# Optimization experiments

Measured on AMD Instinct MI355X. Metric: run time of the kernel, lower is better.

## Reference

```python
import jax, jax.numpy as jnp
import numpy as np
import math

N_STOCKS, SEQ_T, D_FEAT, D_MODEL = 1024, 32, 158, 256
H_T, H_S = 4, 4
MAX_LEN = 100
LN_EPS = 1e-5


def _make_pe():
    # PositionalEncoding buffer, identical to the torch construction
    pos = np.arange(MAX_LEN, dtype=np.float32)[:, None]
    div = np.exp(np.arange(0, D_MODEL, 2, dtype=np.float32) * (-math.log(10000.0) / D_MODEL))
    pe = np.zeros((MAX_LEN, D_MODEL), dtype=np.float32)
    pe[:, 0::2] = np.sin(pos * div)
    pe[:, 1::2] = np.cos(pos * div)
    return jnp.asarray(pe)


def _ln(x, g, b):
    mu = x.mean(-1, keepdims=True)
    var = ((x - mu) ** 2).mean(-1, keepdims=True)
    return (x - mu) / jnp.sqrt(var + LN_EPS) * g + b


def _mha(q, k, v, nhead, scale):
    # q,k,v: [B,S,D]; full (non-causal) attention over S, vectorized over heads
    B, S, D = q.shape
    hd = D // nhead
    qh = q.reshape(B, S, nhead, hd)
    kh = k.reshape(B, S, nhead, hd)
    vh = v.reshape(B, S, nhead, hd)
    scores = jnp.einsum('bqhd,bkhd->bhqk', qh, kh) * scale
    attn = jax.nn.softmax(scores, axis=-1)  # dropout is identity in eval
    out = jnp.einsum('bhqk,bkhd->bqhd', attn, vh)
    return out.reshape(B, S, D)


def _block(x, wq, wk, wv, g1, b1, g2, b2, w1, bb1, w2, bb2, nhead, scale, swap):
    # shared body of TAttention (swap=False, scale=1) / SAttention (swap=True, scale=1/temperature)
    xn = _ln(x, g1, b1)
    q, k, v = xn @ wq, xn @ wk, xn @ wv
    if swap:  # SAttention attends over the stock axis: transpose(0,1)
        q, k, v = q.swapaxes(0, 1), k.swapaxes(0, 1), v.swapaxes(0, 1)
    att = _mha(q, k, v, nhead, scale)
    if swap:
        att = att.swapaxes(0, 1)
    xt = _ln(xn + att, g2, b2)
    ffn = jax.nn.relu(xt @ w1 + bb1) @ w2 + bb2
    return xt + ffn


def _forward(x_enc, emb_w, emb_b, pe,
             t_wq, t_wk, t_wv, t_ln1_g, t_ln1_b, t_ln2_g, t_ln2_b, t_w1, t_b1, t_w2, t_b2,
             s_wq, s_wk, s_wv, s_ln1_g, s_ln1_b, s_ln2_g, s_ln2_b, s_w1, s_b1, s_w2, s_b2,
             ta_w, dec_w, dec_b):
    x = x_enc[0]  # squeeze(dim=0) -> [N, T, d_feat]
    h = x @ emb_w + emb_b + pe[:x.shape[1]]  # embedding + positional encoding
    # TAttention: attention over time axis, NO temperature scaling in source
    h = _block(h, t_wq, t_wk, t_wv, t_ln1_g, t_ln1_b, t_ln2_g, t_ln2_b,
               t_w1, t_b1, t_w2, t_b2, H_T, 1.0, swap=False)
    # SAttention: attention over stock axis, scaled by 1/sqrt(d_model/nhead)
    s_scale = 1.0 / math.sqrt(D_MODEL / H_S)
    h = _block(h, s_wq, s_wk, s_wv, s_ln1_g, s_ln1_b, s_ln2_g, s_ln2_b,
               s_w1, s_b1, s_w2, s_b2, H_S, s_scale, swap=True)
    # TemporalAttention: last-timestep query pooling over T
    hh = h @ ta_w                                  # [N,T,D]
    lam = jnp.einsum('ntd,nd->nt', hh, hh[:, -1, :])
    lam = jax.nn.softmax(lam, axis=1)
    pooled = jnp.einsum('nt,ntd->nd', lam, h)      # matmul(lam[:,None,:], z).squeeze(1)
    return pooled @ dec_w + dec_b                  # [N, 2]


def setup_inputs():
    key = jax.random.key(0)
    ks = iter(jax.random.split(key, 48))
    def w(shape, s=0.02):
        return jax.random.normal(next(ks), shape, dtype=jnp.float32) * s
    D = D_MODEL
    inp = {
        'x_enc': jax.random.normal(next(ks), (1, N_STOCKS, SEQ_T, D_FEAT), jnp.float32),
        'x_mark_enc': jax.random.normal(next(ks), (1, N_STOCKS, SEQ_T, 4), jnp.float32),
        'x_dec': jax.random.normal(next(ks), (1, SEQ_T, D_FEAT), jnp.float32),
        'x_mark_dec': jax.random.normal(next(ks), (1, SEQ_T, 4), jnp.float32),
        'x_tweet': jax.random.randint(next(ks), (1, 128), 0, 30000, dtype=jnp.int32),
        'emb_w': w((D_FEAT, D)), 'emb_b': jnp.zeros((D,), jnp.float32),
        'pe': _make_pe(),
        't_wq': w((D, D)), 't_wk': w((D, D)), 't_wv': w((D, D)),
        't_ln1_g': jnp.ones((D,), jnp.float32), 't_ln1_b': jnp.zeros((D,), jnp.float32),
        't_ln2_g': jnp.ones((D,), jnp.float32), 't_ln2_b': jnp.zeros((D,), jnp.float32),
        't_w1': w((D, D)), 't_b1': jnp.zeros((D,), jnp.float32),
        't_w2': w((D, D)), 't_b2': jnp.zeros((D,), jnp.float32),
        's_wq': w((D, D)), 's_wk': w((D, D)), 's_wv': w((D, D)),
        's_ln1_g': jnp.ones((D,), jnp.float32), 's_ln1_b': jnp.zeros((D,), jnp.float32),
        's_ln2_g': jnp.ones((D,), jnp.float32), 's_ln2_b': jnp.zeros((D,), jnp.float32),
        's_w1': w((D, D)), 's_b1': jnp.zeros((D,), jnp.float32),
        's_w2': w((D, D)), 's_b2': jnp.zeros((D,), jnp.float32),
        'ta_w': w((D, D)),
        'dec_w': w((D, 2)), 'dec_b': jnp.zeros((2,), jnp.float32),
    }
    return inp


def reference(x_enc, x_mark_enc, x_dec, x_mark_dec, x_tweet, emb_w, emb_b, pe,
              t_wq, t_wk, t_wv, t_ln1_g, t_ln1_b, t_ln2_g, t_ln2_b, t_w1, t_b1, t_w2, t_b2,
              s_wq, s_wk, s_wv, s_ln1_g, s_ln1_b, s_ln2_g, s_ln2_b, s_w1, s_b1, s_w2, s_b2,
              ta_w, dec_w, dec_b):
    # x_mark_enc feeds a throwaway fresh Linear whose output is never used;
    # x_dec / x_mark_dec / x_tweet are unused in the source forward.
    pred = _forward(x_enc, emb_w, emb_b, pe,
                    t_wq, t_wk, t_wv, t_ln1_g, t_ln1_b, t_ln2_g, t_ln2_b, t_w1, t_b1, t_w2, t_b2,
                    s_wq, s_wk, s_wv, s_ln1_g, s_ln1_b, s_ln2_g, s_ln2_b, s_w1, s_b1, s_w2, s_b2,
                    ta_w, dec_w, dec_b)
    # (tweet_pred, data_pred, cat_pred, align_loss) all alias data_pred / 0
    return (pred, pred, pred, jnp.float32(0.0))
```

## Files before the change

kernel.cpp:

```cpp
#include <hip/hip_runtime.h>
#include <hip/hip_bf16.h>
#include <math.h>

#define NS 1024
#define ST 32
#define DF 158
#define DM 256
#define KE 192
#define ROWS (NS*ST)
#define SZ ((size_t)ROWS*DM)
#define LN_EPS 1e-5f
#define LOG2E 1.44269504088896f

typedef __attribute__((ext_vector_type(8)))  __bf16 bf16x8;
typedef __attribute__((ext_vector_type(16))) float  f32x16;

__device__ __forceinline__ float wave_sum(float v) {
#pragma unroll
    for (int o = 32; o > 0; o >>= 1) v += __shfl_xor(v, o);
    return v;
}

__device__ __forceinline__ unsigned pkbf(float a, float b) {
    __hip_bfloat16 ha = __float2bfloat16(a), hb = __float2bfloat16(b);
    unsigned short ua, ub;
    __builtin_memcpy(&ua, &ha, 2); __builtin_memcpy(&ub, &hb, 2);
    return (unsigned)ua | ((unsigned)ub << 16);
}

__device__ __forceinline__ unsigned pkbf_fast(float a, float b) {
    unsigned ua = __float_as_uint(a) + 0x8000u;
    unsigned ub = __float_as_uint(b) + 0x8000u;
    return (ua >> 16) | (ub & 0xffff0000u);
}

__device__ __forceinline__ unsigned short sbf(float a) {
    return (unsigned short)((__float_as_uint(a) + 0x8000u) >> 16);
}

__device__ __forceinline__ float2 bf2x(unsigned u) {
    union { unsigned i; float f; } a, b;
    a.i = u << 16; b.i = u & 0xffff0000u;
    return make_float2(a.f, b.f);
}

__device__ __forceinline__ uint4 addpk(uint4 rv, const float* s) {
    float2 f0 = bf2x(rv.x), f1 = bf2x(rv.y), f2 = bf2x(rv.z), f3 = bf2x(rv.w);
    return make_uint4(pkbf_fast(f0.x + s[0], f0.y + s[1]),
                      pkbf_fast(f1.x + s[2], f1.y + s[3]),
                      pkbf_fast(f2.x + s[4], f2.y + s[5]),
                      pkbf_fast(f3.x + s[6], f3.y + s[7]));
}

__device__ __forceinline__ uint4 addbk(uint4 a, uint4 b) {
    float2 a0 = bf2x(a.x), a1 = bf2x(a.y), a2 = bf2x(a.z), a3 = bf2x(a.w);
    float2 b0 = bf2x(b.x), b1 = bf2x(b.y), b2 = bf2x(b.z), b3 = bf2x(b.w);
    return make_uint4(pkbf_fast(a0.x + b0.x, a0.y + b0.y),
                      pkbf_fast(a1.x + b1.x, a1.y + b1.y),
                      pkbf_fast(a2.x + b2.x, a2.y + b2.y),
                      pkbf_fast(a3.x + b3.x, a3.y + b3.y));
}

__global__ __launch_bounds__(256) void cvtx_k(const float* __restrict__ x,
        __hip_bfloat16* __restrict__ xb) {
    int r = blockIdx.x*8 + (threadIdx.x >> 5);
    int c = blockIdx.y*32 + (threadIdx.x & 31);
    float v = (c < DF) ? x[(size_t)r*DF + c] : 0.f;
    xb[(size_t)r*KE + c] = __float2bfloat16(v);
}

struct WPack { const float* s[11]; __hip_bfloat16* d[11]; };

__global__ __launch_bounds__(256) void cvtw_k(WPack wp) {
    const float* W = wp.s[blockIdx.z];
    __hip_bfloat16* Wt = wp.d[blockIdx.z];
    __shared__ float t[64][65];
    int bi = blockIdx.x*64, bj = blockIdx.y*64;
    int r = threadIdx.x >> 2, c0 = (threadIdx.x & 3) * 16;
#pragma unroll
    for (int i = 0; i < 16; i += 4) {
        float4 v = *(const float4*)(W + (size_t)(bi + r)*DM + bj + c0 + i);
        t[r][c0+i+0] = v.x; t[r][c0+i+1] = v.y;
        t[r][c0+i+2] = v.z; t[r][c0+i+3] = v.w;
    }
    __syncthreads();
    unsigned u[8];
#pragma unroll
    for (int i = 0; i < 8; ++i) u[i] = pkbf(t[c0+2*i][r], t[c0+2*i+1][r]);
    __hip_bfloat16* op = Wt + (size_t)(bj + r)*DM + bi + c0;
    *(uint4*)(op)     = make_uint4(u[0], u[1], u[2], u[3]);
    *(uint4*)(op + 8) = make_uint4(u[4], u[5], u[6], u[7]);
}

__global__ __launch_bounds__(192) void cvte_k(const float* __restrict__ W,
        __hip_bfloat16* __restrict__ Wt) {
    int n = blockIdx.x, t = threadIdx.x;
    float v = (t < DF) ? W[(size_t)t*DM + n] : 0.f;
    Wt[(size_t)n*KE + t] = __float2bfloat16(v);
}

__global__ __launch_bounds__(256) void ln_k(const __hip_bfloat16* __restrict__ a,
        const float* __restrict__ g, const float* __restrict__ be,
        __hip_bfloat16* __restrict__ outb) {
    int w = threadIdx.x >> 6, lane = threadIdx.x & 63;
    size_t r = (size_t)blockIdx.x*4 + w;
    uint2 raw = *(const uint2*)(a + r*DM + lane*4);
    float2 v01 = bf2x(raw.x), v23 = bf2x(raw.y);
    float mu = wave_sum(v01.x+v01.y+v23.x+v23.y) * (1.0f/DM);
    float c0 = v01.x-mu, c1 = v01.y-mu, c2 = v23.x-mu, c3 = v23.y-mu;
    float var = wave_sum(c0*c0 + c1*c1 + c2*c2 + c3*c3) * (1.0f/DM);
    float rs = rsqrtf(var + LN_EPS);
    float4 g4 = *(const float4*)(g + lane*4);
    float4 b4 = *(const float4*)(be + lane*4);
    float o0 = c0*rs*g4.x + b4.x, o1 = c1*rs*g4.y + b4.y;
    float o2 = c2*rs*g4.z + b4.z, o3 = c3*rs*g4.w + b4.w;
    *(uint2*)(outb + r*DM + lane*4) = make_uint2(pkbf_fast(o0, o1), pkbf_fast(o2, o3));
}

union __align__(16) GLds {
    struct { __hip_bfloat16 As[64*72]; __hip_bfloat16 Ws[128*72]; } s;
    __hip_bfloat16 Ob[64*136];
};

__global__ __launch_bounds__(256) void mgemm_k(const __hip_bfloat16* __restrict__ A,
        int sA, int nk, const __hip_bfloat16* __restrict__ Wt, int sW,
        const float* __restrict__ bias, const float* __restrict__ pe,
        const __hip_bfloat16* __restrict__ resid, float* __restrict__ Cf,
        __hip_bfloat16* __restrict__ Cb, int relu, int fmt, float scale, int fused) {
    __shared__ GLds gsm;
    const int tid = threadIdx.x;
    const int w = tid >> 6, lane = tid & 63;
    const int uh = lane >> 5, l31 = lane & 31;
    const int wm = (w >> 1)*32, wn = (w & 1)*64;
    const size_t m0 = (size_t)blockIdx.x*64;
    const int n0 = blockIdx.y*128;

    f32x16 acc[2];
#pragma unroll
    for (int nt = 0; nt < 2; ++nt)
#pragma unroll
        for (int r = 0; r < 16; ++r) acc[nt][r] = 0.f;

    const int ra = tid >> 2, ca = (tid & 3)*16;
    const int rw = tid >> 1, cw = (tid & 1)*32;
    const __hip_bfloat16* ap = A  + (m0 + ra)*sA + ca;
    const __hip_bfloat16* wp = Wt + (size_t)(n0 + rw)*sW + cw;
    uint4 pa0 = *(const uint4*)(ap), pa1 = *(const uint4*)(ap + 8);
    uint4 pw0 = *(const uint4*)(wp),      pw1 = *(const uint4*)(wp + 8);
    uint4 pw2 = *(const uint4*)(wp + 16), pw3 = *(const uint4*)(wp + 24);
    for (int kt = 0; kt < nk; ++kt) {
        __syncthreads();
        *(uint4*)&gsm.s.As[ra*72 + ca]     = pa0;
        *(uint4*)&gsm.s.As[ra*72 + ca + 8] = pa1;
        *(uint4*)&gsm.s.Ws[rw*72 + cw]      = pw0;
        *(uint4*)&gsm.s.Ws[rw*72 + cw + 8]  = pw1;
        *(uint4*)&gsm.s.Ws[rw*72 + cw + 16] = pw2;
        *(uint4*)&gsm.s.Ws[rw*72 + cw + 24] = pw3;
        __syncthreads();
        if (kt + 1 < nk) {
            int ko = (kt + 1)*64;
            pa0 = *(const uint4*)(ap + ko);      pa1 = *(const uint4*)(ap + ko + 8);
            pw0 = *(const uint4*)(wp + ko);      pw1 = *(const uint4*)(wp + ko + 8);
            pw2 = *(const uint4*)(wp + ko + 16); pw3 = *(const uint4*)(wp + ko + 24);
        }
#pragma unroll
        for (int ks = 0; ks < 4; ++ks) {
            bf16x8 a0 = *(const bf16x8*)&gsm.s.As[(wm + l31)*72      + ks*16 + uh*8];
            bf16x8 b0 = *(const bf16x8*)&gsm.s.Ws[(wn + l31)*72      + ks*16 + uh*8];
            bf16x8 b1 = *(const bf16x8*)&gsm.s.Ws[(wn + 32 + l31)*72 + ks*16 + uh*8];
            acc[0] = __builtin_amdgcn_mfma_f32_32x32x16_bf16(a0, b0, acc[0], 0, 0, 0);
            acc[1] = __builtin_amdgcn_mfma_f32_32x32x16_bf16(a0, b1, acc[1], 0, 0, 0);
        }
    }

    if (Cf) {
#pragma unroll
        for (int nt = 0; nt < 2; ++nt) {
            int colg = n0 + wn + nt*32 + l31;
            float bz = bias ? bias[colg] : 0.f;
#pragma unroll
            for (int r = 0; r < 16; ++r) {
                size_t mg = m0 + wm + (r & 3) + ((r >> 2) << 3) + 4*uh;
                float v = (acc[nt][r] + bz) * scale;
                if (pe)   v += pe[(mg & 31)*DM + colg];
                if (relu) v = fmaxf(v, 0.f);
                Cf[mg*DM + colg] = v;
            }
        }
    } else {
        __syncthreads();
#pragma unroll
        for (int nt = 0; nt < 2; ++nt) {
            int col = wn + nt*32 + l31;
            int colg = n0 + col;
            int c8  = fused ? (colg & 255) : colg;
            float sc = (fused && (colg >> 8)) ? 1.0f : scale;
            float bz = bias ? bias[c8] : 0.f;
#pragma unroll
            for (int r = 0; r < 16; ++r) {
                int mrow = wm + (r & 3) + ((r >> 2) << 3) + 4*uh;
                float v = (acc[nt][r] + bz) * sc;
                if (pe)   v += pe[((m0 + mrow) & 31)*DM + c8];
                if (relu) v = fmaxf(v, 0.f);
                *(unsigned short*)&gsm.Ob[mrow*136 + col] = sbf(v);
            }
        }
        __syncthreads();
        int m = tid >> 2;
        size_t mg = m0 + m;
#pragma unroll
        for (int i = 0; i < 4; ++i) {
            int ncol = ((tid & 3) + 4*i)*8;
            uint4 val = *(const uint4*)&gsm.Ob[m*136 + ncol];
            int colg = n0 + ncol;
            int seg = fused ? (colg >> 8) : 0;
            int c8  = fused ? (colg & 255) : colg;
            if (resid) val = addbk(val, *(const uint4*)(resid + mg*DM + c8));
            size_t oidx;
            if (fmt == 1)
                oidx = (size_t)((mg & 31)*4 + (c8 >> 6))*65536 + (mg >> 5)*64 + (c8 & 63);
            else if (fmt == 2)
                oidx = ((size_t)(c8 >> 6)*NS + (mg >> 5))*2048 + (mg & 31)*64 + (c8 & 63);
            else
                oidx = mg*DM + c8;
            *(uint4*)&(Cb + (size_t)seg*SZ)[oidx] = val;
        }
    }
}

union __align__(16) WLds { __hip_bfloat16 vt[64*40]; float ob[32*68]; };

__global__ __launch_bounds__(256) void attnT_k(const __hip_bfloat16* __restrict__ Q,
        const __hip_bfloat16* __restrict__ K, const __hip_bfloat16* __restrict__ V,
        const __hip_bfloat16* __restrict__ R, const float* __restrict__ g,
        const float* __restrict__ be, __hip_bfloat16* __restrict__ O) {
    __shared__ WLds sm4[4];
    __shared__ float redS[32][8];
    __shared__ float redQ[32][8];
    const int n = blockIdx.x;
    const int w = threadIdx.x >> 6, lane = threadIdx.x & 63;
    const int uh = lane >> 5, l31 = lane & 31;
    const size_t base = ((size_t)w*NS + n)*2048;

    bf16x8 kf[4], qf[4];
#pragma unroll
    for (int s = 0; s < 4; ++s) {
        kf[s] = *(const bf16x8*)(K + base + l31*64 + s*16 + uh*8);
        qf[s] = *(const bf16x8*)(Q + base + l31*64 + s*16 + uh*8);
    }
    __hip_bfloat16* vt = sm4[w].vt;
#pragma unroll
    for (int i = 0; i < 2; ++i) {
        int c = lane*2 + i;
        int dg = c >> 3, tg = c & 7;
        const ushort* vp = (const ushort*)(V + base + (tg*4)*64 + dg*4);
        ushort4 s0 = *(const ushort4*)(vp);
        ushort4 s1 = *(const ushort4*)(vp + 64);
        ushort4 s2 = *(const ushort4*)(vp + 128);
        ushort4 s3 = *(const ushort4*)(vp + 192);
        *(uint2*)&vt[(dg*4+0)*40 + tg*4] = make_uint2((unsigned)s0.x | ((unsigned)s1.x<<16),
                                                      (unsigned)s2.x | ((unsigned)s3.x<<16));
        *(uint2*)&vt[(dg*4+1)*40 + tg*4] = make_uint2((unsigned)s0.y | ((unsigned)s1.y<<16),
                                                      (unsigned)s2.y | ((unsigned)s3.y<<16));
        *(uint2*)&vt[(dg*4+2)*40 + tg*4] = make_uint2((unsigned)s0.z | ((unsigned)s1.z<<16),
                                                      (unsigned)s2.z | ((unsigned)s3.z<<16));
        *(uint2*)&vt[(dg*4+3)*40 + tg*4] = make_uint2((unsigned)s0.w | ((unsigned)s1.w<<16),
                                                      (unsigned)s2.w | ((unsigned)s3.w<<16));
    }

    f32x16 sa;
#pragma unroll
    for (int r = 0; r < 16; ++r) sa[r] = 0.f;
    sa = __builtin_amdgcn_mfma_f32_32x32x16_bf16(kf[0], qf[0], sa, 0, 0, 0);
    sa = __builtin_amdgcn_mfma_f32_32x32x16_bf16(kf[1], qf[1], sa, 0, 0, 0);
    sa = __builtin_amdgcn_mfma_f32_32x32x16_bf16(kf[2], qf[2], sa, 0, 0, 0);
    sa = __builtin_amdgcn_mfma_f32_32x32x16_bf16(kf[3], qf[3], sa, 0, 0, 0);

    float p[16], l = 0.f;
#pragma unroll
    for (int r = 0; r < 16; ++r) { p[r] = __builtin_amdgcn_exp2f(sa[r]); l += p[r]; }
    l += __shfl_xor(l, 32);

    bf16x8 pf[2];
#pragma unroll
    for (int s = 0; s < 2; ++s) {
        unsigned A0 = pkbf_fast(p[8*s+0], p[8*s+1]);
        unsigned A1 = pkbf_fast(p[8*s+2], p[8*s+3]);
        unsigned B0 = pkbf_fast(p[8*s+4], p[8*s+5]);
        unsigned B1 = pkbf_fast(p[8*s+6], p[8*s+7]);
        unsigned xA0 = (unsigned)__shfl_xor((int)A0, 32);
        unsigned xA1 = (unsigned)__shfl_xor((int)A1, 32);
        unsigned xB0 = (unsigned)__shfl_xor((int)B0, 32);
        unsigned xB1 = (unsigned)__shfl_xor((int)B1, 32);
        union { uint4 i; bf16x8 v; } cv;
        cv.i = make_uint4(uh ? xB0 : A0, uh ? xB1 : A1,
                          uh ? B0 : xA0, uh ? B1 : xA1);
        pf[s] = cv.v;
    }

    f32x16 oa[2];
#pragma unroll
    for (int c = 0; c < 2; ++c) {
#pragma unroll
        for (int r = 0; r < 16; ++r) oa[c][r] = 0.f;
        bf16x8 v0 = *(const bf16x8*)&vt[(c*32 + l31)*40 + uh*8];
        bf16x8 v1 = *(const bf16x8*)&vt[(c*32 + l31)*40 + 16 + uh*8];
        oa[c] = __builtin_amdgcn_mfma_f32_32x32x16_bf16(v0, pf[0], oa[c], 0, 0, 0);
        oa[c] = __builtin_amdgcn_mfma_f32_32x32x16_bf16(v1, pf[1], oa[c], 0, 0, 0);
    }

    float invl = 1.0f / l;
    float* ob = sm4[w].ob;
#pragma unroll
    for (int c = 0; c < 2; ++c)
#pragma unroll
        for (int r = 0; r < 16; ++r) {
            int d = (r & 3) + ((r >> 2) << 3) + 4*uh + 32*c;
            ob[l31*68 + d] = oa[c][r] * invl;
        }
    int t = lane >> 1, d0 = (lane & 1)*32;
    size_t gi = ((size_t)n*ST + t)*DM + w*64 + d0;
    float ps = 0.f, pq = 0.f;
#pragma unroll
    for (int i = 0; i < 4; ++i) {
        uint4 rv = *(const uint4*)(R + gi + 8*i);
        float* s = &ob[t*68 + d0 + 8*i];
        float2 f0 = bf2x(rv.x), f1 = bf2x(rv.y), f2 = bf2x(rv.z), f3 = bf2x(rv.w);
        float v0 = f0.x + s[0], v1 = f0.y + s[1], v2 = f1.x + s[2], v3 = f1.y + s[3];
        float v4 = f2.x + s[4], v5 = f2.y + s[5], v6 = f3.x + s[6], v7 = f3.y + s[7];
        s[0] = v0; s[1] = v1; s[2] = v2; s[3] = v3;
        s[4] = v4; s[5] = v5; s[6] = v6; s[7] = v7;
        ps += v0+v1+v2+v3+v4+v5+v6+v7;
        pq += v0*v0+v1*v1+v2*v2+v3*v3+v4*v4+v5*v5+v6*v6+v7*v7;
    }
    redS[t][w*2 + (lane & 1)] = ps;
    redQ[t][w*2 + (lane & 1)] = pq;
    __syncthreads();
    float s8 = 0.f, q8 = 0.f;
#pragma unroll
    for (int i = 0; i < 8; ++i) { s8 += redS[t][i]; q8 += redQ[t][i]; }
    float mu = s8*(1.0f/DM);
    float var = q8*(1.0f/DM) - mu*mu;
    float rcp = rsqrtf(var + LN_EPS);
#pragma unroll
    for (int i = 0; i < 4; ++i) {
        const float* s = &ob[t*68 + d0 + 8*i];
        int cg = w*64 + d0 + 8*i;
        float4 g0 = *(const float4*)(g + cg),  g1 = *(const float4*)(g + cg + 4);
        float4 b0 = *(const float4*)(be + cg), b1 = *(const float4*)(be + cg + 4);
        float o0 = (s[0]-mu)*rcp*g0.x + b0.x, o1 = (s[1]-mu)*rcp*g0.y + b0.y;
        float o2 = (s[2]-mu)*rcp*g0.z + b0.z, o3 = (s[3]-mu)*rcp*g0.w + b0.w;
        float o4 = (s[4]-mu)*rcp*g1.x + b1.x, o5 = (s[5]-mu)*rcp*g1.y + b1.y;
        float o6 = (s[6]-mu)*rcp*g1.z + b1.z, o7 = (s[7]-mu)*rcp*g1.w + b1.w;
        *(uint4*)(O + gi + 8*i) = make_uint4(pkbf_fast(o0, o1), pkbf_fast(o2, o3),
                                             pkbf_fast(o4, o5), pkbf_fast(o6, o7));
    }
}

union __align__(16) LdsS {
    struct { __hip_bfloat16 K[64*72]; __hip_bfloat16 Vt[64*72]; } s;
    float Ob[4][32*68];
};

__global__ __launch_bounds__(256) void attnS_k(const __hip_bfloat16* __restrict__ Qb,
        const __hip_bfloat16* __restrict__ Kb, const __hip_bfloat16* __restrict__ Vb,
        const __hip_bfloat16* __restrict__ R, __hip_bfloat16* __restrict__ O) {
    __shared__ LdsS sm;
    const int tt = blockIdx.x, h = blockIdx.y, qt = blockIdx.z;
    const int tid = threadIdx.x;
    const int w = tid >> 6, lane = tid & 63;
    const int uh = lane >> 5, l31 = lane & 31;
    const size_t hb = (size_t)(tt*4 + h)*65536;

    bf16x8 qf[4];
    {
        const __hip_bfloat16* qp = Qb + hb + (size_t)(qt*128 + w*32 + l31)*64 + 8*uh;
        qf[0] = *(const bf16x8*)(qp);
        qf[1] = *(const bf16x8*)(qp + 16);
        qf[2] = *(const bf16x8*)(qp + 32);
        qf[3] = *(const bf16x8*)(qp + 48);
    }

    f32x16 oa[2];
#pragma unroll
    for (int c = 0; c < 2; ++c)
#pragma unroll
        for (int r = 0; r < 16; ++r) oa[c][r] = 0.f;
    float lrun = 0.f;

    for (int kt = 0; kt < 16; ++kt) {
        __syncthreads();
        {
            const __hip_bfloat16* kb = Kb + hb + (size_t)kt*4096;
#pragma unroll
            for (int i = 0; i < 2; ++i) {
                int c = tid*2 + i;
                int j = c >> 3, col = (c & 7)*8;
                *(uint4*)&sm.s.K[j*72 + col] = *(const uint4*)(kb + c*8);
            }
        }
        {
            int j0 = (tid & 15)*4, cb = (tid >> 4)*4;
            const ushort* vp = (const ushort*)(Vb + hb + (size_t)(kt*64 + j0)*64 + cb);
            ushort4 s0 = *(const ushort4*)(vp);
            ushort4 s1 = *(const ushort4*)(vp + 64);
            ushort4 s2 = *(const ushort4*)(vp + 128);
            ushort4 s3 = *(const ushort4*)(vp + 192);
            *(uint2*)&sm.s.Vt[(cb+0)*72 + j0] = make_uint2((unsigned)s0.x | ((unsigned)s1.x<<16),
                                                           (unsigned)s2.x | ((unsigned)s3.x<<16));
            *(uint2*)&sm.s.Vt[(cb+1)*72 + j0] = make_uint2((unsigned)s0.y | ((unsigned)s1.y<<16),
                                                           (unsigned)s2.y | ((unsigned)s3.y<<16));
            *(uint2*)&sm.s.Vt[(cb+2)*72 + j0] = make_uint2((unsigned)s0.z | ((unsigned)s1.z<<16),
                                                           (unsigned)s2.z | ((unsigned)s3.z<<16));
            *(uint2*)&sm.s.Vt[(cb+3)*72 + j0] = make_uint2((unsigned)s0.w | ((unsigned)s1.w<<16),
                                                           (unsigned)s2.w | ((unsigned)s3.w<<16));
        }
        __syncthreads();

        f32x16 sa[2];
#pragma unroll
        for (int ct = 0; ct < 2; ++ct) {
            f32x16 a2;
#pragma unroll
            for (int r = 0; r < 16; ++r) a2[r] = 0.f;
            const __hip_bfloat16* kb = &sm.s.K[(ct*32 + l31)*72 + 8*uh];
            a2 = __builtin_amdgcn_mfma_f32_32x32x16_bf16(*(const bf16x8*)(kb +  0), qf[0], a2, 0, 0, 0);
            a2 = __builtin_amdgcn_mfma_f32_32x32x16_bf16(*(const bf16x8*)(kb + 16), qf[1], a2, 0, 0, 0);
            a2 = __builtin_amdgcn_mfma_f32_32x32x16_bf16(*(const bf16x8*)(kb + 32), qf[2], a2, 0, 0, 0);
            a2 = __builtin_amdgcn_mfma_f32_32x32x16_bf16(*(const bf16x8*)(kb + 48), qf[3], a2, 0, 0, 0);
            sa[ct] = a2;
        }

        float p[32];
        float rs = 0.f;
#pragma unroll
        for (int ct = 0; ct < 2; ++ct)
#pragma unroll
            for (int r = 0; r < 16; ++r) {
                float e = __builtin_amdgcn_exp2f(sa[ct][r]);
                p[ct*16 + r] = e;
                rs += e;
            }
        rs += __shfl_xor(rs, 32);
        lrun += rs;

        bf16x8 bfr[4];
#pragma unroll
        for (int q = 0; q < 4; ++q) {
            int ct = q >> 1, b = (q & 1) << 3;
            unsigned A0 = pkbf_fast(p[ct*16+b+0], p[ct*16+b+1]);
            unsigned A1 = pkbf_fast(p[ct*16+b+2], p[ct*16+b+3]);
            unsigned B0 = pkbf_fast(p[ct*16+b+4], p[ct*16+b+5]);
            unsigned B1 = pkbf_fast(p[ct*16+b+6], p[ct*16+b+7]);
            unsigned xA0 = (unsigned)__shfl_xor((int)A0, 32);
            unsigned xA1 = (unsigned)__shfl_xor((int)A1, 32);
            unsigned xB0 = (unsigned)__shfl_xor((int)B0, 32);
            unsigned xB1 = (unsigned)__shfl_xor((int)B1, 32);
            union { uint4 i; bf16x8 v; } cv;
            cv.i = make_uint4(uh ? xB0 : A0, uh ? xB1 : A1,
                              uh ? B0 : xA0, uh ? B1 : xA1);
            bfr[q] = cv.v;
        }

#pragma unroll
        for (int c = 0; c < 2; ++c) {
            const __hip_bfloat16* vb = &sm.s.Vt[(c*32 + l31)*72 + 8*uh];
            oa[c] = __builtin_amdgcn_mfma_f32_32x32x16_bf16(*(const bf16x8*)(vb +  0), bfr[0], oa[c], 0, 0, 0);
            oa[c] = __builtin_amdgcn_mfma_f32_32x32x16_bf16(*(const bf16x8*)(vb + 16), bfr[1], oa[c], 0, 0, 0);
            oa[c] = __builtin_amdgcn_mfma_f32_32x32x16_bf16(*(const bf16x8*)(vb + 32), bfr[2], oa[c], 0, 0, 0);
            oa[c] = __builtin_amdgcn_mfma_f32_32x32x16_bf16(*(const bf16x8*)(vb + 48), bfr[3], oa[c], 0, 0, 0);
        }
    }

    __syncthreads();
    float invl = 1.0f / lrun;
    float* ob = sm.Ob[w];
#pragma unroll
    for (int c = 0; c < 2; ++c)
#pragma unroll
        for (int r = 0; r < 16; ++r) {
            int d = (r & 3) + ((r >> 2) << 3) + 4*uh + 32*c;
            ob[l31*68 + d] = oa[c][r] * invl;
        }
#pragma unroll
    for (int pp = 0; pp < 2; ++pp) {
        int qr = pp*16 + (lane >> 2);
        int dc = (lane & 3) << 4;
        size_t gi = ((size_t)(qt*128 + w*32 + qr)*ST + tt)*DM + h*64 + dc;
#pragma unroll
        for (int i = 0; i < 2; ++i) {
            uint4 rv = *(const uint4*)(R + gi + 8*i);
            *(uint4*)(O + gi + 8*i) = addpk(rv, &ob[qr*68 + dc + 8*i]);
        }
    }
}

__global__ __launch_bounds__(256) void final_k(const __hip_bfloat16* __restrict__ H,
        const float* __restrict__ HH, const float* __restrict__ dw,
        const float* __restrict__ db, float* __restrict__ out) {
    int n = blockIdx.x, d = threadIdx.x;
    int w = d >> 6, lane = d & 63;
    __shared__ float lam[ST];
    __shared__ float red[8];
    const float* hh = HH + (size_t)n*ST*DM;
    float4 qd = *(const float4*)(hh + 31*DM + lane*4);
#pragma unroll
    for (int i = 0; i < 8; ++i) {
        int t = w*8 + i;
        float4 h4 = *(const float4*)(hh + t*DM + lane*4);
        float s = wave_sum(h4.x*qd.x + h4.y*qd.y + h4.z*qd.z + h4.w*qd.w);
        if (lane == 0) lam[t] = s;
    }
    __syncthreads();
    float mx = -1e30f;
#pragma unroll
    for (int t = 0; t < ST; ++t) mx = fmaxf(mx, lam[t]);
    float sum = 0.f;
#pragma unroll
    for (int t = 0; t < ST; ++t) sum += __expf(lam[t]-mx);
    float acc = 0.f;
    const __hip_bfloat16* hrow = H + (size_t)n*ST*DM;
#pragma unroll
    for (int t = 0; t < ST; ++t)
        acc += __expf(lam[t]-mx) * __bfloat162float(hrow[t*DM + d]);
    acc /= sum;
    float p0 = wave_sum(acc * dw[2*d+0]);
    float p1 = wave_sum(acc * dw[2*d+1]);
    if (lane == 0) { red[w] = p0; red[4 + w] = p1; }
    __syncthreads();
    if (d == 0) {
        float r0 = red[0]+red[1]+red[2]+red[3] + db[0];
        float r1 = red[4]+red[5]+red[6]+red[7] + db[1];
        out[(size_t)n*2+0] = r0;           out[(size_t)n*2+1] = r1;
        out[2048 + (size_t)n*2+0] = r0;    out[2048 + (size_t)n*2+1] = r1;
        out[4096 + (size_t)n*2+0] = r0;    out[4096 + (size_t)n*2+1] = r1;
        if (n == 0) out[6144] = 0.f;
    }
}

extern "C" void kernel_launch(void* const* d_in, const int* in_sizes, int n_in,
                              void* d_out, int out_size, void* d_ws, size_t ws_size,
                              hipStream_t stream) {
    const float* x     = (const float*)d_in[0];
    const float* emb_w = (const float*)d_in[5];
    const float* emb_b = (const float*)d_in[6];
    const float* pe    = (const float*)d_in[7];
    const float* t_g1  = (const float*)d_in[11];
    const float* t_b1  = (const float*)d_in[12];
    const float* t_g2  = (const float*)d_in[13];
    const float* t_b2  = (const float*)d_in[14];
    const float* t_bb1 = (const float*)d_in[16];
    const float* t_bb2 = (const float*)d_in[18];
    const float* s_g1  = (const float*)d_in[22];
    const float* s_b1  = (const float*)d_in[23];
    const float* s_g2  = (const float*)d_in[24];
    const float* s_b2  = (const float*)d_in[25];
    const float* s_bb1 = (const float*)d_in[27];
    const float* s_bb2 = (const float*)d_in[29];
    const float* dec_w = (const float*)d_in[31];
    const float* dec_b = (const float*)d_in[32];
    float* out = (float*)d_out;

    float* F0 = (float*)d_ws;
    __hip_bfloat16* B0 = (__hip_bfloat16*)(F0 + SZ);
    __hip_bfloat16* B1 = B0 + SZ;
    __hip_bfloat16* B2 = B1 + SZ;
    __hip_bfloat16* B3 = B2 + SZ;
    __hip_bfloat16* B4 = B3 + SZ;
    __hip_bfloat16* WT  = B4 + SZ;
    __hip_bfloat16* WTE = WT + (size_t)11*DM*DM;
    __hip_bfloat16* XB  = WTE + (size_t)DM*KE;

    cvtx_k<<<dim3(ROWS/8, KE/32), 256, 0, stream>>>(x, XB);
    WPack wp;
    const int widx[11] = {8, 9, 10, 15, 17, 19, 20, 21, 26, 28, 30};
    for (int i = 0; i < 11; ++i) {
        wp.s[i] = (const float*)d_in[widx[i]];
        wp.d[i] = WT + (size_t)i*DM*DM;
    }
    cvtw_k<<<dim3(4, 4, 11), 256, 0, stream>>>(wp);
    cvte_k<<<DM, 192, 0, stream>>>(emb_w, WTE);

    dim3 gg(ROWS/64, 2);
    dim3 gq(ROWS/64, 6);
    __hip_bfloat16* WqT = WT;
    __hip_bfloat16* W1  = WT + (size_t)3*DM*DM;
    __hip_bfloat16* W2  = WT + (size_t)4*DM*DM;
    __hip_bfloat16* SWq = WT + (size_t)5*DM*DM;
    __hip_bfloat16* SW1 = WT + (size_t)8*DM*DM;
    __hip_bfloat16* SW2 = WT + (size_t)9*DM*DM;
    __hip_bfloat16* WTA = WT + (size_t)10*DM*DM;

    mgemm_k<<<gg, 256, 0, stream>>>(XB, KE, 3, WTE, KE, emb_b, pe, nullptr, nullptr, B0, 0, 0, 1.f, 0);
    ln_k<<<ROWS/4, 256, 0, stream>>>(B0, t_g1, t_b1, B1);
    mgemm_k<<<gq, 256, 0, stream>>>(B1, 256, 4, WqT, 256, nullptr, nullptr, nullptr, nullptr, B2, 0, 2, LOG2E, 1);
    attnT_k<<<NS, 256, 0, stream>>>(B2, B3, B4, B1, t_g2, t_b2, B1);
    mgemm_k<<<gg, 256, 0, stream>>>(B1, 256, 4, W1, 256, t_bb1, nullptr, nullptr, nullptr, B2, 1, 0, 1.f, 0);
    mgemm_k<<<gg, 256, 0, stream>>>(B2, 256, 4, W2, 256, t_bb2, nullptr, B1, nullptr, B0, 0, 0, 1.f, 0);
    ln_k<<<ROWS/4, 256, 0, stream>>>(B0, s_g1, s_b1, B1);
    mgemm_k<<<gq, 256, 0, stream>>>(B1, 256, 4, SWq, 256, nullptr, nullptr, nullptr, nullptr, B2, 0, 1, 0.125f*LOG2E, 1);
    attnS_k<<<dim3(32, 4, 8), 256, 0, stream>>>(B2, B3, B4, B1, B0);
    ln_k<<<ROWS/4, 256, 0, stream>>>(B0, s_g2, s_b2, B1);
    mgemm_k<<<gg, 256, 0, stream>>>(B1, 256, 4, SW1, 256, s_bb1, nullptr, nullptr, nullptr, B2, 1, 0, 1.f, 0);
    mgemm_k<<<gg, 256, 0, stream>>>(B2, 256, 4, SW2, 256, s_bb2, nullptr, B1, nullptr, B0, 0, 0, 1.f, 0);
    mgemm_k<<<gg, 256, 0, stream>>>(B0, 256, 4, WTA, 256, nullptr, nullptr, nullptr, F0, nullptr, 0, 0, 1.f, 0);
    final_k<<<NS, 256, 0, stream>>>(B0, F0, dec_w, dec_b, out);
}
```

Measured before the change: 395.3 us.

## Replace temporal-attention projection GEMM with precomputed W·Wᵀ applied to last step

Instead of projecting all 32 time steps through ta_w in a full GEMM and dotting each with the projected last step, the score h_t·(W Wᵀ h_31) is computed. A small kernel forms M = W Wᵀ once per call, and final_k computes y = M h_31 per stock before dotting it with the raw hidden states. This removes a full ROWS×256×256 GEMM and its float output buffer. The cost is a per-stock 256×256 matvec in final_k and a change in rounding order.

```diff
diff --git a/kernel.cpp b/kernel.cpp
--- a/kernel.cpp
+++ b/kernel.cpp
@@ -97,6 +97,19 @@
     int n = blockIdx.x, t = threadIdx.x;
     float v = (t < DF) ? W[(size_t)t*DM + n] : 0.f;
     Wt[(size_t)n*KE + t] = __float2bfloat16(v);
+}
+
+__global__ __launch_bounds__(256) void wwt_k(const __hip_bfloat16* __restrict__ T,
+        float* __restrict__ M) {
+    int a = blockIdx.x, b = threadIdx.x;
+    __shared__ float ta[DM];
+    ta[b] = __bfloat162float(T[(size_t)b*DM + a]);
+    __syncthreads();
+    float m = 0.f;
+#pragma unroll 4
+    for (int k = 0; k < DM; ++k)
+        m += ta[k] * __bfloat162float(T[(size_t)k*DM + b]);
+    M[(size_t)a*DM + b] = m;
 }
 
 __global__ __launch_bounds__(256) void ln_k(const __hip_bfloat16* __restrict__ a,
@@ -125,7 +138,7 @@
 __global__ __launch_bounds__(256) void mgemm_k(const __hip_bfloat16* __restrict__ A,
         int sA, int nk, const __hip_bfloat16* __restrict__ Wt, int sW,
         const float* __restrict__ bias, const float* __restrict__ pe,
-        const __hip_bfloat16* __restrict__ resid, float* __restrict__ Cf,
+        const __hip_bfloat16* __restrict__ resid,
         __hip_bfloat16* __restrict__ Cb, int relu, int fmt, float scale, int fused) {
     __shared__ GLds gsm;
     const int tid = threadIdx.x;
@@ -173,58 +186,42 @@
         }
     }
 
-    if (Cf) {
-#pragma unroll
-        for (int nt = 0; nt < 2; ++nt) {
-            int colg = n0 + wn + nt*32 + l31;
-            float bz = bias ? bias[colg] : 0.f;
-#pragma unroll
-            for (int r = 0; r < 16; ++r) {
-                size_t mg = m0 + wm + (r & 3) + ((r >> 2) << 3) + 4*uh;
-                float v = (acc[nt][r] + bz) * scale;
-                if (pe)   v += pe[(mg & 31)*DM + colg];
-                if (relu) v = fmaxf(v, 0.f);
-                Cf[mg*DM + colg] = v;
-            }
-        }
-    } else {
-        __syncthreads();
-#pragma unroll
-        for (int nt = 0; nt < 2; ++nt) {
-            int col = wn + nt*32 + l31;
-            int colg = n0 + col;
-            int c8  = fused ? (colg & 255) : colg;
-            float sc = (fused && (colg >> 8)) ? 1.0f : scale;
-            float bz = bias ? bias[c8] : 0.f;
-#pragma unroll
-            for (int r = 0; r < 16; ++r) {
-                int mrow = wm + (r & 3) + ((r >> 2) << 3) + 4*uh;
-                float v = (acc[nt][r] + bz) * sc;
-                if (pe)   v += pe[((m0 + mrow) & 31)*DM + c8];
-                if (relu) v = fmaxf(v, 0.f);
-                *(unsigned short*)&gsm.Ob[mrow*136 + col] = sbf(v);
-            }
-        }
-        __syncthreads();
-        int m = tid >> 2;
-        size_t mg = m0 + m;
-#pragma unroll
-        for (int i = 0; i < 4; ++i) {
-            int ncol = ((tid & 3) + 4*i)*8;
-            uint4 val = *(const uint4*)&gsm.Ob[m*136 + ncol];
-            int colg = n0 + ncol;
-            int seg = fused ? (colg >> 8) : 0;
-            int c8  = fused ? (colg & 255) : colg;
-            if (resid) val = addbk(val, *(const uint4*)(resid + mg*DM + c8));
-            size_t oidx;
-            if (fmt == 1)
-                oidx = (size_t)((mg & 31)*4 + (c8 >> 6))*65536 + (mg >> 5)*64 + (c8 & 63);
-            else if (fmt == 2)
-                oidx = ((size_t)(c8 >> 6)*NS + (mg >> 5))*2048 + (mg & 31)*64 + (c8 & 63);
-            else
-                oidx = mg*DM + c8;
-            *(uint4*)&(Cb + (size_t)seg*SZ)[oidx] = val;
-        }
+    __syncthreads();
+#pragma unroll
+    for (int nt = 0; nt < 2; ++nt) {
+        int col = wn + nt*32 + l31;
+        int colg = n0 + col;
+        int c8  = fused ? (colg & 255) : colg;
+        float sc = (fused && (colg >> 8)) ? 1.0f : scale;
+        float bz = bias ? bias[c8] : 0.f;
+#pragma unroll
+        for (int r = 0; r < 16; ++r) {
+            int mrow = wm + (r & 3) + ((r >> 2) << 3) + 4*uh;
+            float v = (acc[nt][r] + bz) * sc;
+            if (pe)   v += pe[((m0 + mrow) & 31)*DM + c8];
+            if (relu) v = fmaxf(v, 0.f);
+            *(unsigned short*)&gsm.Ob[mrow*136 + col] = sbf(v);
+        }
+    }
+    __syncthreads();
+    int m = tid >> 2;
+    size_t mg = m0 + m;
+#pragma unroll
+    for (int i = 0; i < 4; ++i) {
+        int ncol = ((tid & 3) + 4*i)*8;
+        uint4 val = *(const uint4*)&gsm.Ob[m*136 + ncol];
+        int colg = n0 + ncol;
+        int seg = fused ? (colg >> 8) : 0;
+        int c8  = fused ? (colg & 255) : colg;
+        if (resid) val = addbk(val, *(const uint4*)(resid + mg*DM + c8));
+        size_t oidx;
+        if (fmt == 1)
+            oidx = (size_t)((mg & 31)*4 + (c8 >> 6))*65536 + (mg >> 5)*64 + (c8 & 63);
+        else if (fmt == 2)
+            oidx = ((size_t)(c8 >> 6)*NS + (mg >> 5))*2048 + (mg & 31)*64 + (c8 & 63);
+        else
+            oidx = mg*DM + c8;
+        *(uint4*)&(Cb + (size_t)seg*SZ)[oidx] = val;
     }
 }
 
@@ -496,19 +493,29 @@
 }
 
 __global__ __launch_bounds__(256) void final_k(const __hip_bfloat16* __restrict__ H,
-        const float* __restrict__ HH, const float* __restrict__ dw,
+        const float* __restrict__ M, const float* __restrict__ dw,
         const float* __restrict__ db, float* __restrict__ out) {
     int n = blockIdx.x, d = threadIdx.x;
     int w = d >> 6, lane = d & 63;
+    __shared__ float h31s[DM];
+    __shared__ float ys[DM];
     __shared__ float lam[ST];
     __shared__ float red[8];
-    const float* hh = HH + (size_t)n*ST*DM;
-    float4 qd = *(const float4*)(hh + 31*DM + lane*4);
+    const __hip_bfloat16* hrow = H + (size_t)n*ST*DM;
+    h31s[d] = __bfloat162float(hrow[31*DM + d]);
+    __syncthreads();
+    float y = 0.f;
+#pragma unroll 4
+    for (int k = 0; k < DM; ++k) y += M[(size_t)k*DM + d] * h31s[k];
+    ys[d] = y;
+    __syncthreads();
 #pragma unroll
     for (int i = 0; i < 8; ++i) {
         int t = w*8 + i;
-        float4 h4 = *(const float4*)(hh + t*DM + lane*4);
-        float s = wave_sum(h4.x*qd.x + h4.y*qd.y + h4.z*qd.z + h4.w*qd.w);
+        uint2 hv = *(const uint2*)(hrow + t*DM + lane*4);
+        float2 a = bf2x(hv.x), b = bf2x(hv.y);
+        float4 yv = *(const float4*)(&ys[lane*4]);
+        float s = wave_sum(a.x*yv.x + a.y*yv.y + b.x*yv.z + b.y*yv.w);
         if (lane == 0) lam[t] = s;
     }
     __syncthreads();
@@ -519,7 +526,6 @@
 #pragma unroll
     for (int t = 0; t < ST; ++t) sum += __expf(lam[t]-mx);
     float acc = 0.f;
-    const __hip_bfloat16* hrow = H + (size_t)n*ST*DM;
 #pragma unroll
     for (int t = 0; t < ST; ++t)
         acc += __expf(lam[t]-mx) * __bfloat162float(hrow[t*DM + d]);
@@ -561,8 +567,8 @@
     const float* dec_b = (const float*)d_in[32];
     float* out = (float*)d_out;
 
-    float* F0 = (float*)d_ws;
-    __hip_bfloat16* B0 = (__hip_bfloat16*)(F0 + SZ);
+    float* MW = (float*)d_ws;
+    __hip_bfloat16* B0 = (__hip_bfloat16*)(MW + SZ);
     __hip_bfloat16* B1 = B0 + SZ;
     __hip_bfloat16* B2 = B1 + SZ;
     __hip_bfloat16* B3 = B2 + SZ;
@@ -591,18 +597,19 @@
     __hip_bfloat16* SW2 = WT + (size_t)9*DM*DM;
     __hip_bfloat16* WTA = WT + (size_t)10*DM*DM;
 
-    mgemm_k<<<gg, 256, 0, stream>>>(XB, KE, 3, WTE, KE, emb_b, pe, nullptr, nullptr, B0, 0, 0, 1.f, 0);
+    wwt_k<<<DM, 256, 0, stream>>>(WTA, MW);
+
+    mgemm_k<<<gg, 256, 0, stream>>>(XB, KE, 3, WTE, KE, emb_b, pe, nullptr, B0, 0, 0, 1.f, 0);
     ln_k<<<ROWS/4, 256, 0, stream>>>(B0, t_g1, t_b1, B1);
-    mgemm_k<<<gq, 256, 0, stream>>>(B1, 256, 4, WqT, 256, nullptr, nullptr, nullptr, nullptr, B2, 0, 2, LOG2E, 1);
+    mgemm_k<<<gq, 256, 0, stream>>>(B1, 256, 4, WqT, 256, nullptr, nullptr, nullptr, B2, 0, 2, LOG2E, 1);
     attnT_k<<<NS, 256, 0, stream>>>(B2, B3, B4, B1, t_g2, t_b2, B1);
-    mgemm_k<<<gg, 256, 0, stream>>>(B1, 256, 4, W1, 256, t_bb1, nullptr, nullptr, nullptr, B2, 1, 0, 1.f, 0);
-    mgemm_k<<<gg, 256, 0, stream>>>(B2, 256, 4, W2, 256, t_bb2, nullptr, B1, nullptr, B0, 0, 0, 1.f, 0);
+    mgemm_k<<<gg, 256, 0, stream>>>(B1, 256, 4, W1, 256, t_bb1, nullptr, nullptr, B2, 1, 0, 1.f, 0);
+    mgemm_k<<<gg, 256, 0, stream>>>(B2, 256, 4, W2, 256, t_bb2, nullptr, B1, B0, 0, 0, 1.f, 0);
     ln_k<<<ROWS/4, 256, 0, stream>>>(B0, s_g1, s_b1, B1);
-    mgemm_k<<<gq, 256, 0, stream>>>(B1, 256, 4, SWq, 256, nullptr, nullptr, nullptr, nullptr, B2, 0, 1, 0.125f*LOG2E, 1);
+    mgemm_k<<<gq, 256, 0, stream>>>(B1, 256, 4, SWq, 256, nullptr, nullptr, nullptr, B2, 0, 1, 0.125f*LOG2E, 1);
     attnS_k<<<dim3(32, 4, 8), 256, 0, stream>>>(B2, B3, B4, B1, B0);
     ln_k<<<ROWS/4, 256, 0, stream>>>(B0, s_g2, s_b2, B1);
-    mgemm_k<<<gg, 256, 0, stream>>>(B1, 256, 4, SW1, 256, s_bb1, nullptr, nullptr, nullptr, B2, 1, 0, 1.f, 0);
-    mgemm_k<<<gg, 256, 0, stream>>>(B2, 256, 4, SW2, 256, s_bb2, nullptr, B1, nullptr, B0, 0, 0, 1.f, 0);
-    mgemm_k<<<gg, 256, 0, stream>>>(B0, 256, 4, WTA, 256, nullptr, nullptr, nullptr, F0, nullptr, 0, 0, 1.f, 0);
-    final_k<<<NS, 256, 0, stream>>>(B0, F0, dec_w, dec_b, out);
-}
+    mgemm_k<<<gg, 256, 0, stream>>>(B1, 256, 4, SW1, 256, s_bb1, nullptr, nullptr, B2, 1, 0, 1.f, 0);
+    mgemm_k<<<gg, 256, 0, stream>>>(B2, 256, 4, SW2, 256, s_bb2, nullptr, B1, B0, 0, 0, 1.f, 0);
+    final_k<<<NS, 256, 0, stream>>>(B0, MW, dec_w, dec_b, out);
+}
```

After: 404.6 us. +2.3%, slower.
